# Optimization experiments

Measured on AMD Instinct MI355X. Metric: run time of the kernel, lower is better.

The kernel has to match this reference:

```python
import jax, jax.numpy as jnp
import numpy as np
import math

T_STEPS = 100      # diffusion steps
TED = 16           # time_embed_dim
NODE_C = 4         # node_num_classes
EDGE_C = 2         # edge_num_classes
HID = 64           # hidden_dim
H = 4              # nhead
B = 256            # graphs per batch
NPG = 64           # nodes per graph
DEG = 8            # avg out-degree
N = B * NPG
E = N * DEG
IN_CH = NODE_C + TED  # 20


def sinusoidal_embedding(t_vec, dim):
    # t_vec: [1] float. Matches get_sinusoidal_embedding for even dim.
    half = dim // 2
    scale = math.log(10000.0) / (half - 1)
    freqs = jnp.exp(-jnp.arange(half, dtype=jnp.float32) * scale)  # [half]
    emb = t_vec[:, None] * freqs[None, :]                          # [1, half]
    return jnp.concatenate([jnp.sin(emb), jnp.cos(emb)], axis=1)   # [1, dim]


def transformer_conv(x, src, dst, Wq, bq, Wk, bk, Wv, bv, Ws, bs):
    # PyG TransformerConv, concat=False (mean over heads), root_weight=True,
    # beta=False, no edge features, dropout=0 (eval).
    n = x.shape[0]
    q = (x @ Wq + bq).reshape(n, H, HID)
    k = (x @ Wk + bk).reshape(n, H, HID)
    v = (x @ Wv + bv).reshape(n, H, HID)
    # attention logits per edge, softmax over incoming edges of each dst node
    logits = jnp.sum(q[dst] * k[src], axis=-1) / math.sqrt(HID)    # [E, H]
    lmax = jax.ops.segment_max(logits, dst, num_segments=n)       # [n, H]
    ex = jnp.exp(logits - lmax[dst])                              # [E, H]
    denom = jax.ops.segment_sum(ex, dst, num_segments=n)          # [n, H]
    attn = ex / jnp.where(denom == 0, 1.0, denom)[dst]            # [E, H]
    msg = v[src] * attn[:, :, None]                               # [E, H, HID]
    agg = jax.ops.segment_sum(msg, dst, num_segments=n)           # [n, H, HID]
    return agg.mean(axis=1) + x @ Ws + bs                         # [n, HID]


def setup_inputs() -> dict:
    key = jax.random.key(0)
    ks = jax.random.split(key, 32)

    # node features: random one-hot labels
    labels = jax.random.randint(ks[0], (N,), 0, NODE_C)
    x = jax.nn.one_hot(labels, NODE_C, dtype=jnp.float32)

    # per-graph random edges (kept within each graph via offsets)
    src_l = jax.random.randint(ks[1], (B, NPG * DEG), 0, NPG)
    dst_l = jax.random.randint(ks[2], (B, NPG * DEG), 0, NPG)
    off = (jnp.arange(B) * NPG)[:, None]
    edge_index = jnp.stack([(src_l + off).reshape(-1), (dst_l + off).reshape(-1)]).astype(jnp.int64)

    batch = jnp.repeat(jnp.arange(B, dtype=jnp.int64), NPG)

    def lin(k, fin, fout):
        kw, kb = jax.random.split(k)
        W = jax.random.normal(kw, (fin, fout), jnp.float32) / math.sqrt(fin)
        b = jax.random.normal(kb, (fout,), jnp.float32) * 0.01
        return W, b

    W_time, b_time = lin(ks[3], TED, TED)
    Wq1, bq1 = lin(ks[4], IN_CH, H * HID)
    Wk1, bk1 = lin(ks[5], IN_CH, H * HID)
    Wv1, bv1 = lin(ks[6], IN_CH, H * HID)
    Ws1, bs1 = lin(ks[7], IN_CH, HID)
    Wq2, bq2 = lin(ks[8], HID, H * HID)
    Wk2, bk2 = lin(ks[9], HID, H * HID)
    Wv2, bv2 = lin(ks[10], HID, H * HID)
    Ws2, bs2 = lin(ks[11], HID, HID)
    W_node, b_node = lin(ks[12], HID, NODE_C)
    W_e1, b_e1 = lin(ks[13], 2 * HID, HID)
    W_e2, b_e2 = lin(ks[14], HID, EDGE_C)

    return dict(x=x, edge_index=edge_index, batch=batch, t=50,
                W_time=W_time, b_time=b_time,
                Wq1=Wq1, bq1=bq1, Wk1=Wk1, bk1=bk1, Wv1=Wv1, bv1=bv1, Ws1=Ws1, bs1=bs1,
                Wq2=Wq2, bq2=bq2, Wk2=Wk2, bk2=bk2, Wv2=Wv2, bv2=bv2, Ws2=Ws2, bs2=bs2,
                W_node=W_node, b_node=b_node, W_e1=W_e1, b_e1=b_e1, W_e2=W_e2, b_e2=b_e2)


def reference(x, edge_index, batch, t,
              W_time, b_time,
              Wq1, bq1, Wk1, bk1, Wv1, bv1, Ws1, bs1,
              Wq2, bq2, Wk2, bk2, Wv2, bv2, Ws2, bs2,
              W_node, b_node, W_e1, b_e1, W_e2, b_e2):
    src, dst = edge_index[0], edge_index[1]

    # time embedding: sinusoidal(t/T) -> Linear -> broadcast to all nodes
    t_vec = jnp.asarray([t], jnp.float32) / T_STEPS
    temb = sinusoidal_embedding(t_vec, TED) @ W_time + b_time      # [1, TED]
    temb = jnp.broadcast_to(temb, (x.shape[0], TED))
    x_in = jnp.concatenate([x, temb], axis=1)                      # [N, 20]

    h = jax.nn.relu(transformer_conv(x_in, src, dst, Wq1, bq1, Wk1, bk1, Wv1, bv1, Ws1, bs1))
    h = jax.nn.relu(transformer_conv(h, src, dst, Wq2, bq2, Wk2, bk2, Wv2, bv2, Ws2, bs2))

    node_logits = h @ W_node + b_node                              # [N, 4]

    # to_dense_batch with equal-sized graphs == reshape; vectorized edge MLP
    hd = h.reshape(B, NPG, HID)
    pair = jnp.concatenate([
        jnp.broadcast_to(hd[:, :, None, :], (B, NPG, NPG, HID)),
        jnp.broadcast_to(hd[:, None, :, :], (B, NPG, NPG, HID)),
    ], axis=-1)                                                    # [B, n, n, 2*HID]
    e_hidden = jax.nn.relu(pair @ W_e1 + b_e1)
    edge_logits = e_hidden @ W_e2 + b_e2                           # [B, n, n, 2]
    return node_logits, edge_logits
```

## Files before the change

### kernel.cpp

```cpp
#include <hip/hip_runtime.h>
#include <math.h>

constexpr int EPG  = 512;
constexpr int ETOT = 131072;

constexpr size_t TAB_Q  = 0;
constexpr size_t TAB_K  = 1024;
constexpr size_t TAB_V  = 2048;
constexpr size_t TAB_S  = 3072;
constexpr size_t TAB_LG = 3328;
constexpr size_t TAB_VV = 3392;
constexpr size_t OFF_H2P = 65536;

constexpr int PK_V_HI   = 0;
constexpr int PK_V_LO   = 16384;
constexpr int PK_S_HI   = 32768;
constexpr int PK_S_LO   = 36864;
constexpr int PK_E1T_HI = 40960;
constexpr int PK_E1T_LO = 45056;
constexpr int PK_E1B_HI = 49152;
constexpr int PK_E1B_LO = 53248;
constexpr int PK_M_HI   = 57344;
constexpr int PK_M_LO   = 73728;

typedef short bf16x8 __attribute__((ext_vector_type(8)));
typedef float f32x4  __attribute__((ext_vector_type(4)));

__device__ __forceinline__ short f2bf(float x) {
    unsigned u = __float_as_uint(x);
    u = (u + 0x7fffu + ((u >> 16) & 1u)) >> 16;
    return (short)u;
}
__device__ __forceinline__ float bf2f(short h) {
    return __uint_as_float(((unsigned)(unsigned short)h) << 16);
}
__device__ __forceinline__ void splt(float x, short& hi, short& lo) {
    hi = f2bf(x);
    lo = f2bf(x - bf2f(hi));
}

__device__ __forceinline__ f32x4 mfma3(bf16x8 ah, bf16x8 al, bf16x8 bh, bf16x8 bl, f32x4 c) {
    c = __builtin_amdgcn_mfma_f32_16x16x32_bf16(ah, bh, c, 0, 0, 0);
    c = __builtin_amdgcn_mfma_f32_16x16x32_bf16(ah, bl, c, 0, 0, 0);
    c = __builtin_amdgcn_mfma_f32_16x16x32_bf16(al, bh, c, 0, 0, 0);
    return c;
}

__device__ __forceinline__ bf16x8 ldsfrag(const short* p, int rowb, int kb, int lane) {
    return *(const bf16x8*)&p[(rowb + (lane & 15)) * 72 + kb + ((lane >> 4) << 3)];
}
__device__ __forceinline__ bf16x8 gpfrag(const short* p, int colb, int kb, int lane) {
    return *(const bf16x8*)&p[((colb + (lane & 15)) << 6) + kb + ((lane >> 4) << 3)];
}

__device__ __forceinline__ void unpack8(const unsigned* p, bf16x8& hv, bf16x8& lv) {
    uint4 a = *(const uint4*)p;
    uint4 b = *(const uint4*)(p + 4);
    unsigned u[8] = {a.x, a.y, a.z, a.w, b.x, b.y, b.z, b.w};
    bf16x8 h, l;
    #pragma unroll
    for (int i = 0; i < 8; i++) { h[i] = (short)(u[i] >> 16); l[i] = (short)(u[i] & 0xffffu); }
    hv = h; lv = l;
}

__global__ __launch_bounds__(256) void k_tabprep(
    const int* __restrict__ t_ptr,
    const float* __restrict__ Wt,  const float* __restrict__ bt,
    const float* __restrict__ Wq1, const float* __restrict__ bq1,
    const float* __restrict__ Wk1, const float* __restrict__ bk1,
    const float* __restrict__ Wv1, const float* __restrict__ bv1,
    const float* __restrict__ Ws1, const float* __restrict__ bs1,
    const float* __restrict__ Wq2, const float* __restrict__ bq2,
    const float* __restrict__ Wk2, const float* __restrict__ Wv2,
    const float* __restrict__ Ws2, const float* __restrict__ We1,
    float* __restrict__ ws, short* __restrict__ wsh)
{
    const int t = threadIdx.x, b = blockIdx.x;
    if (b < 112) {
        const float* src; int N; int dhi; int nb;
        if (b < 64)      { src = Wv2;           N = 256; dhi = PK_V_HI;   nb = b; }
        else if (b < 80) { src = Ws2;           N = 64;  dhi = PK_S_HI;   nb = b - 64; }
        else if (b < 96) { src = We1;           N = 64;  dhi = PK_E1T_HI; nb = b - 80; }
        else             { src = We1 + 64 * 64; N = 64;  dhi = PK_E1B_HI; nb = b - 96; }
        int dlo = dhi + N * 64;
        int n = nb * 4 + (t >> 6), kk = t & 63;
        float v = src[(size_t)kk * N + n];
        short hi, lo; splt(v, hi, lo);
        wsh[dhi + n * 64 + kk] = hi;
        wsh[dlo + n * 64 + kk] = lo;
// ... 8 lines not shown
            wk[r][a] = Wk2[(size_t)r * 256 + h * 64 + a];
        }
        __syncthreads();
        int m = t >> 2, k0 = (t & 3) * 16;
        for (int kk = k0; kk < k0 + 16; kk++) {
            float acc = 0.f;
            for (int a = 0; a < 64; a++) acc += wq[kk][a] * wk[m][a];
            acc *= 0.125f;
            short hi, lo; splt(acc, hi, lo);
            wsh[PK_M_HI + h * 4096 + m * 64 + kk] = hi;
            wsh[PK_M_LO + h * 4096 + m * 64 + kk] = lo;
        }
        if (t < 64) {
            float acc = 0.f;
            for (int a = 0; a < 64; a++) acc += wk[t][a] * bq2[h * 64 + a];
            ws[TAB_VV + h * 64 + t] = 0.125f * acc;
        }
        return;
    }
    __shared__ float se[16], temb[16];
    __shared__ float q1t[4][256], k1t[4][256], v1t[4][256], s1t[4][64];
    if (t < 8) {
        float tv = (float)(*t_ptr) * 0.01f;
        float scale = logf(10000.0f) / 7.0f;
        float e = tv * expf(-(float)t * scale);
        se[t]     = sinf(e);
        se[t + 8] = cosf(e);
    }
    __syncthreads();
    if (t < 16) {
        float acc = bt[t];
// ... 23 lines not shown
    }
    __syncthreads();
    for (int idx = t; idx < 1024; idx += 256) {
        int c = idx >> 8, o = idx & 255;
        ws[TAB_Q + idx] = q1t[c][o];
        ws[TAB_K + idx] = k1t[c][o];
        ws[TAB_V + idx] = v1t[c][o];
    }
    ws[TAB_S + t] = s1t[t >> 6][t & 63];
    if (t < 64) {
        int cd = t >> 4, cs = (t >> 2) & 3, h = t & 3;
        float acc = 0.f;
        for (int d = 0; d < 64; d++) acc += q1t[cd][h * 64 + d] * k1t[cs][h * 64 + d];
        ws[TAB_LG + t] = acc * 0.125f;
    }
}

__global__ __launch_bounds__(512, 4) void k_main(
    const float* __restrict__ x, const int* __restrict__ ei,
    const float* __restrict__ ws, const short* __restrict__ wsh,
    const float* __restrict__ bv, const float* __restrict__ bsk,
    unsigned* __restrict__ h2p)
{
    __shared__ __align__(16) char smem[61184];
    short* hHi  = (short*)(smem);
    short* hLo  = (short*)(smem + 9216);
    short* GHi  = (short*)(smem + 18432);
    short* GLo  = (short*)(smem + 23040);
    short* VtHi = (short*)(smem + 27648);
    short* VtLo = (short*)(smem + 36864);
    float* SPf  = (float*)(smem + 46080);
    int*   Cc   = (int*)(smem + 54784);
    float* wcol = (float*)(smem + 59136);
    float* vvs  = (float*)(smem + 60160);
    float* v1t    = (float*)(smem + 27648);
    float* s1t    = (float*)(smem + 31744);
    float* lgs    = (float*)(smem + 32768);
    float* alphaF = (float*)(smem + 33024);
    int*   cls    = (int*)(smem + 37120);
    int*   cnt4   = (int*)(smem + 37376);

    const int g   = blockIdx.x >> 1;
    const int r0  = (blockIdx.x & 1) * 32;
    const int t   = threadIdx.x;
    const int lane = t & 63, w = t >> 6;
    const int rb  = (w & 1) * 16;
    const int cb  = (w >> 1) * 16;
    const int db  = (w & 3) * 16;
    const int jb0 = (w >> 2) * 32;
    const int lg4 = ((lane >> 4) << 2);
    const int lg8 = ((lane >> 4) << 3);
    const int l15 = lane & 15;
    const int row8 = t >> 3;
    const int d08  = (t & 7) * 8;

    for (int i = t; i < 1024; i += 512) v1t[i] = ws[TAB_V + i];
    if (t < 256) s1t[t] = ws[TAB_S + t];
    if (t < 64)  lgs[t] = ws[TAB_LG + t];
    if (t < 256) vvs[t] = ws[TAB_VV + t];
    if (t < 64) {
        const float* xr = x + (size_t)(g * 64 + t) * 4;
        int c = 0;
        if (xr[1] > 0.5f) c = 1;
        if (xr[2] > 0.5f) c = 2;
        if (xr[3] > 0.5f) c = 3;
        cls[t] = c;
    }
    if (t < 256) cnt4[t] = 0;
    for (int i = t; i < 1056; i += 512) Cc[i] = 0;
    __syncthreads();

    {
        int ge = g * EPG + t;
        int ls = ei[ge] - g * 64;
        int ld = ei[ETOT + ge] - g * 64;
        atomicAdd(&cnt4[ld * 4 + cls[ls]], 1);
        int lr = ld - r0;
        if ((unsigned)lr < 32u) {
            int idx = lr * 66 + ls;
            atomicAdd(&Cc[idx >> 1], 1 << ((idx & 1) * 16));
        }
    }
    __syncthreads();

    if (t < 256) {
        int n = t >> 2, h = t & 3;
        int cd = cls[n];
        int   c[4]; float l[4];
        #pragma unroll
        for (int cc = 0; cc < 4; cc++) {
            c[cc] = cnt4[n * 4 + cc];
            l[cc] = lgs[cd * 16 + cc * 4 + h];
        }
        float m = -1e30f;
        #pragma unroll
        for (int cc = 0; cc < 4; cc++) if (c[cc] > 0) m = fmaxf(m, l[cc]);
        float e[4]; float den = 0.f;
        #pragma unroll
        for (int cc = 0; cc < 4; cc++) {
            e[cc] = (c[cc] > 0) ? (float)c[cc] * __expf(l[cc] - m) : 0.f;
            den += e[cc];
        }
        float inv = (den > 0.f) ? 0.25f / den : 0.f;
        #pragma unroll
        for (int cc = 0; cc < 4; cc++) alphaF[n * 16 + h * 4 + cc] = e[cc] * inv;
    }
    __syncthreads();

    {
        int cd = cls[row8];
        float a[16];
        #pragma unroll
        for (int q = 0; q < 16; q++) a[q] = alphaF[row8 * 16 + q];
        #pragma unroll
        for (int jj = 0; jj < 8; jj++) {
            int d = d08 + jj;
            float acc = s1t[cd * 64 + d];
            #pragma unroll
            for (int h = 0; h < 4; h++)
                #pragma unroll
                for (int c = 0; c < 4; c++)
                    acc += a[h * 4 + c] * v1t[c * 256 + h * 64 + d];
            float o = fmaxf(acc, 0.f);
            short hi, lo; splt(o, hi, lo);
            hHi[row8 * 72 + d] = hi;
            hLo[row8 * 72 + d] = lo;
        }
    }
    __syncthreads();

    bf16x8 AhQ0 = ldsfrag(hHi, r0 + rb, 0, lane),  AhQ1 = ldsfrag(hHi, r0 + rb, 32, lane);
    bf16x8 AlQ0 = ldsfrag(hLo, r0 + rb, 0, lane),  AlQ1 = ldsfrag(hLo, r0 + rb, 32, lane);
    bf16x8 sb0h = ldsfrag(hHi, cb, 0, lane),  sb0l = ldsfrag(hLo, cb, 0, lane);
    bf16x8 sb1h = ldsfrag(hHi, cb, 32, lane), sb1l = ldsfrag(hLo, cb, 32, lane);

    if (t < 256) {
        int j = t >> 2, hh = t & 3;
        float acc = 0.f;
        #pragma unroll 8
        for (int k = 0; k < 64; k++)
            acc += (bf2f(hHi[j * 72 + k]) + bf2f(hLo[j * 72 + k])) * vvs[hh * 64 + k];
        wcol[hh * 64 + j] = acc;
    }

    f32x4 skacc = {0.f, 0.f, 0.f, 0.f};
    {
        bf16x8 s0h = gpfrag(wsh + PK_S_HI, cb, 0, lane),  s0l = gpfrag(wsh + PK_S_LO, cb, 0, lane);
        bf16x8 s1h = gpfrag(wsh + PK_S_HI, cb, 32, lane), s1l = gpfrag(wsh + PK_S_LO, cb, 32, lane);
        skacc = mfma3(AhQ0, AlQ0, s0h, s0l, skacc);
        skacc = mfma3(AhQ1, AlQ1, s1h, s1l, skacc);
        float bb = bsk[cb + l15];
        #pragma unroll
        for (int r = 0; r < 4; r++) skacc[r] += bb;
    }

    float hacc[4] = {0.f, 0.f, 0.f, 0.f};
    #pragma unroll 1
    for (int h = 0; h < 4; h++) {
        const short* pmh = wsh + PK_M_HI + h * 4096;
        const short* pml = wsh + PK_M_LO + h * 4096;
        bf16x8 m0h = gpfrag(pmh, cb, 0, lane),  m0l = gpfrag(pml, cb, 0, lane);
        bf16x8 m1h = gpfrag(pmh, cb, 32, lane), m1l = gpfrag(pml, cb, 32, lane);
        int gc0 = h * 64 + db;
        bf16x8 va0h = gpfrag(wsh + PK_V_HI, gc0, 0, lane),  va0l = gpfrag(wsh + PK_V_LO, gc0, 0, lane);
        bf16x8 va1h = gpfrag(wsh + PK_V_HI, gc0, 32, lane), va1l = gpfrag(wsh + PK_V_LO, gc0, 32, lane);
        float4 bv4 = *(const float4*)&bv[gc0 + lg4];
        bf16x8 hb00 = ldsfrag(hHi, jb0, 0, lane),       hb00l = ldsfrag(hLo, jb0, 0, lane);
        bf16x8 hb01 = ldsfrag(hHi, jb0, 32, lane),      hb01l = ldsfrag(hLo, jb0, 32, lane);
        bf16x8 hb10 = ldsfrag(hHi, jb0 + 16, 0, lane),  hb10l = ldsfrag(hLo, jb0 + 16, 0, lane);
        bf16x8 hb11 = ldsfrag(hHi, jb0 + 16, 32, lane), hb11l = ldsfrag(hLo, jb0 + 16, 32, lane);

        {
            f32x4 ga = {0.f, 0.f, 0.f, 0.f};
            ga = mfma3(AhQ0, AlQ0, m0h, m0l, ga);
            ga = mfma3(AhQ1, AlQ1, m1h, m1l, ga);
            int cc = cb + l15;
            #pragma unroll
            for (int r = 0; r < 4; r++) {
                short hi, lo; splt(ga[r], hi, lo);
                GHi[(rb + lg4 + r) * 72 + cc] = hi;
                GLo[(rb + lg4 + r) * 72 + cc] = lo;
            }
        }
        {
            f32x4 vt0 = {0.f, 0.f, 0.f, 0.f}, vt1 = {0.f, 0.f, 0.f, 0.f};
            vt0 = mfma3(va0h, va0l, hb00, hb00l, vt0);
            vt0 = mfma3(va1h, va1l, hb01, hb01l, vt0);
            vt1 = mfma3(va0h, va0l, hb10, hb10l, vt1);
            vt1 = mfma3(va1h, va1l, hb11, hb11l, vt1);
            #pragma unroll
            for (int r = 0; r < 4; r++) {
                int rr = (db + lg4 + r) * 72;
                short hi, lo;
                splt(vt0[r] + bv4[r], hi, lo);
                VtHi[rr + jb0 + l15] = hi;      VtLo[rr + jb0 + l15] = lo;
                splt(vt1[r] + bv4[r], hi, lo);
                VtHi[rr + jb0 + 16 + l15] = hi; VtLo[rr + jb0 + 16 + l15] = lo;
            }
        }
        __syncthreads();

        bf16x8 vb0h = ldsfrag(VtHi, cb, 0, lane),  vb0l = ldsfrag(VtLo, cb, 0, lane);
        bf16x8 vb1h = ldsfrag(VtHi, cb, 32, lane), vb1l = ldsfrag(VtLo, cb, 32, lane);
        {
            bf16x8 g0h = ldsfrag(GHi, rb, 0, lane),  g0l = ldsfrag(GLo, rb, 0, lane);
            bf16x8 g1h = ldsfrag(GHi, rb, 32, lane), g1l = ldsfrag(GLo, rb, 32, lane);
            f32x4 s = {0.f, 0.f, 0.f, 0.f};
            s = mfma3(g0h, g0l, sb0h, sb0l, s);
            s = mfma3(g1h, g1l, sb1h, sb1l, s);
            int cc = cb + l15;
            #pragma unroll
            for (int r = 0; r < 4; r++)
                SPf[(rb + lg4 + r) * 68 + cc] = s[r];
        }
        __syncthreads();

        {
            const int lr = rb + l15;
            float sv[16];
            {
                float4 a0 = *(const float4*)&SPf[lr * 68 + lg8];
                float4 a1 = *(const float4*)&SPf[lr * 68 + lg8 + 4];
                float4 a2 = *(const float4*)&SPf[lr * 68 + 32 + lg8];
                float4 a3 = *(const float4*)&SPf[lr * 68 + 32 + lg8 + 4];
                sv[0]=a0.x; sv[1]=a0.y; sv[2]=a0.z; sv[3]=a0.w;
                sv[4]=a1.x; sv[5]=a1.y; sv[6]=a1.z; sv[7]=a1.w;
                sv[8]=a2.x; sv[9]=a2.y; sv[10]=a2.z; sv[11]=a2.w;
                sv[12]=a3.x; sv[13]=a3.y; sv[14]=a3.z; sv[15]=a3.w;
            }
            int cv[16];
            #pragma unroll
            for (int e = 0; e < 8; e++) {
                int i0 = lr * 66 + lg8 + e;
                int i1 = lr * 66 + 32 + lg8 + e;
                cv[e]     = (Cc[i0 >> 1] >> ((i0 & 1) * 16)) & 0xffff;
                cv[8 + e] = (Cc[i1 >> 1] >> ((i1 & 1) * 16)) & 0xffff;
                sv[e]     += wcol[h * 64 + lg8 + e];
                sv[8 + e] += wcol[h * 64 + 32 + lg8 + e];
            }
            float m = -1e30f;
            #pragma unroll
            for (int e = 0; e < 16; e++) if (cv[e] > 0) m = fmaxf(m, sv[e]);
            m = fmaxf(m, __shfl_xor(m, 16));
            m = fmaxf(m, __shfl_xor(m, 32));
            float den = 0.f; float p[16];
            #pragma unroll
            for (int e = 0; e < 16; e++) {
                p[e] = (cv[e] > 0) ? (float)cv[e] * __expf(sv[e] - m) : 0.f;
                den += p[e];
            }
            den += __shfl_xor(den, 16);
            den += __shfl_xor(den, 32);
            float inv = (den > 0.f) ? 1.f / den : 0.f;
            bf16x8 pa0h, pa0l, pa1h, pa1l;
            #pragma unroll
            for (int e = 0; e < 8; e++) {
                short hi, lo;
                splt(p[e] * inv, hi, lo);      pa0h[e] = hi; pa0l[e] = lo;
                splt(p[8 + e] * inv, hi, lo);  pa1h[e] = hi; pa1l[e] = lo;
            }
            f32x4 pv = {0.f, 0.f, 0.f, 0.f};
            pv = mfma3(pa0h, pa0l, vb0h, vb0l, pv);
            pv = mfma3(pa1h, pa1l, vb1h, vb1l, pv);
            #pragma unroll
            for (int r = 0; r < 4; r++) hacc[r] += pv[r];
        }
        __syncthreads();
    }

    {
        int cc = cb + l15;
        #pragma unroll
        for (int r = 0; r < 4; r++) {
            float v = fmaxf(0.25f * hacc[r] + skacc[r], 0.f);
            short hi, lo; splt(v, hi, lo);
            unsigned u = ((unsigned)(unsigned short)hi << 16) | (unsigned short)(unsigned short)lo;
            h2p[(size_t)(g * 64 + r0 + rb + lg4 + r) * 64 + cc] = u;
        }
    }
}

__global__ __launch_bounds__(512, 4) void k_edge(
    const short* __restrict__ wsh, const unsigned* __restrict__ h2g,
    const float* __restrict__ Wn, const float* __restrict__ bn,
    const float* __restrict__ be1, const float* __restrict__ We2,
    const float* __restrict__ be2, float* __restrict__ out)
{
    __shared__ __align__(16) char smem[45056];
    unsigned* h2P = (unsigned*)(smem);
    float* Af   = (float*)(smem + 17408);
    float* BTf  = (float*)(smem + 26112);
    float* WnS  = (float*)(smem + 43520);
    float* w2s  = (float*)(smem + 44544);

    const int g  = blockIdx.x >> 1;
    const int r0 = (blockIdx.x & 1) * 32;
    const int t  = threadIdx.x;
    const int lane = t & 63, w = t >> 6;
    const int rowbF = (w & 3) * 16, chF = w >> 2;
    const int rbQ = (w & 1) * 16,   cqQ = (w >> 1) * 16;
    const int lg4 = ((lane >> 4) << 2);
    const int lg8 = ((lane >> 4) << 3);
    const int l15 = lane & 15;

    {
        int row = t >> 3, c8 = (t & 7) * 8;
        uint4 a = *(const uint4*)&h2g[(size_t)(g * 64 + row) * 64 + c8];
        uint4 b = *(const uint4*)&h2g[(size_t)(g * 64 + row) * 64 + c8 + 4];
        *(uint4*)&h2P[row * 68 + c8]     = a;
        *(uint4*)&h2P[row * 68 + c8 + 4] = b;
    }
    if (t < 256) WnS[t] = Wn[t];
    if (t < 128) w2s[(t & 1) * 64 + (t >> 1)] = We2[t];
    __syncthreads();

    {
        bf16x8 e0h = gpfrag(wsh + PK_E1T_HI, cqQ, 0, lane),  e0l = gpfrag(wsh + PK_E1T_LO, cqQ, 0, lane);
        bf16x8 e1h = gpfrag(wsh + PK_E1T_HI, cqQ, 32, lane), e1l = gpfrag(wsh + PK_E1T_LO, cqQ, 32, lane);
        bf16x8 aq0, lq0, aq1, lq1;
        unpack8(&h2P[(r0 + rbQ + l15) * 68 + lg8], aq0, lq0);
        unpack8(&h2P[(r0 + rbQ + l15) * 68 + 32 + lg8], aq1, lq1);
        f32x4 aa = {0.f, 0.f, 0.f, 0.f};
        aa = mfma3(aq0, lq0, e0h, e0l, aa);
        aa = mfma3(aq1, lq1, e1h, e1l, aa);
        float bev = be1[cqQ + l15];
        #pragma unroll
        for (int r = 0; r < 4; r++)
            Af[(rbQ + lg4 + r) * 68 + cqQ + l15] = aa[r] + bev;
    }
    {
        bf16x8 af0, lf0, af1, lf1;
        unpack8(&h2P[(rowbF + l15) * 68 + lg8], af0, lf0);
        unpack8(&h2P[(rowbF + l15) * 68 + 32 + lg8], af1, lf1);
        #pragma unroll
        for (int ct = 0; ct < 2; ct++) {
            int colb = chF * 32 + ct * 16;
            bf16x8 b0h = gpfrag(wsh + PK_E1B_HI, colb, 0, lane),  b0l = gpfrag(wsh + PK_E1B_LO, colb, 0, lane);
            bf16x8 b1h = gpfrag(wsh + PK_E1B_HI, colb, 32, lane), b1l = gpfrag(wsh + PK_E1B_LO, colb, 32, lane);
            f32x4 bb = {0.f, 0.f, 0.f, 0.f};
            bb = mfma3(af0, lf0, b0h, b0l, bb);
            bb = mfma3(af1, lf1, b1h, b1l, bb);
            int cc = colb + l15;
            #pragma unroll
            for (int r = 0; r < 4; r++)
                BTf[cc * 68 + rowbF + lg4 + r] = bb[r];
        }
    }
    if (t < 128) {
        int n = t >> 2, c = t & 3;
        float acc = bn[c];
        #pragma unroll 8
        for (int k = 0; k < 64; k++) {
            unsigned u = h2P[(r0 + n) * 68 + k];
            float val = __uint_as_float(u & 0xffff0000u) + __uint_as_float(u << 16);
            acc += val * WnS[k * 4 + c];
        }
        out[(size_t)(g * 64 + r0 + n) * 4 + c] = acc;
    }
    __syncthreads();

    {
        const int wv = t >> 6, j = t & 63;
        float e0[4], e1[4];
        const float cb0 = be2[0], cb1 = be2[1];
        #pragma unroll
        for (int ii = 0; ii < 4; ii++) { e0[ii] = cb0; e1[ii] = cb1; }
        for (int kb = 0; kb < 4; kb++) {
            const int k0 = kb * 16;
            float bj[16], wa[16], wb[16];
            #pragma unroll
            for (int q = 0; q < 16; q++) {
                bj[q] = BTf[(k0 + q) * 68 + j];
                wa[q] = w2s[k0 + q];
                wb[q] = w2s[64 + k0 + q];
            }
            #pragma unroll
            for (int ii = 0; ii < 4; ii++) {
                const float* ar = &Af[(wv * 4 + ii) * 68 + k0];
                #pragma unroll
                for (int q = 0; q < 16; q += 4) {
                    float4 a4 = *(const float4*)(ar + q);
                    float s;
                    s = fmaxf(a4.x + bj[q + 0], 0.f); e0[ii] += s * wa[q + 0]; e1[ii] += s * wb[q + 0];
                    s = fmaxf(a4.y + bj[q + 1], 0.f); e0[ii] += s * wa[q + 1]; e1[ii] += s * wb[q + 1];
                    s = fmaxf(a4.z + bj[q + 2], 0.f); e0[ii] += s * wa[q + 2]; e1[ii] += s * wb[q + 2];
                    s = fmaxf(a4.w + bj[q + 3], 0.f); e0[ii] += s * wa[q + 3]; e1[ii] += s * wb[q + 3];
                }
            }
        }
        float2* oe = (float2*)(out + 65536);
        #pragma unroll
        for (int ii = 0; ii < 4; ii++)
            oe[(size_t)(g * 64 + r0 + wv * 4 + ii) * 64 + j] = make_float2(e0[ii], e1[ii]);
    }
}

extern "C" void kernel_launch(void* const* d_in, const int* in_sizes, int n_in,
                              void* d_out, int out_size, void* d_ws, size_t ws_size,
                              hipStream_t stream)
{
    const float* x    = (const float*)d_in[0];
    const int*   ei   = (const int*)d_in[1];
    const int*   tptr = (const int*)d_in[3];
    const float* Wt   = (const float*)d_in[4];
    const float* bt   = (const float*)d_in[5];
    const float* Wq1  = (const float*)d_in[6];
    const float* bq1  = (const float*)d_in[7];
    const float* Wk1  = (const float*)d_in[8];
// ... 10 lines not shown
    const float* Ws2  = (const float*)d_in[20];
    const float* bs2  = (const float*)d_in[21];
    const float* Wn   = (const float*)d_in[22];
    const float* bn   = (const float*)d_in[23];
    const float* We1  = (const float*)d_in[24];
    const float* be1  = (const float*)d_in[25];
    const float* We2  = (const float*)d_in[26];
    const float* be2  = (const float*)d_in[27];

    float* ws  = (float*)d_ws;
    short* wsh = (short*)(ws + 4096);
    unsigned* h2p = (unsigned*)(ws + OFF_H2P);
    float* out = (float*)d_out;

    k_tabprep<<<117, 256, 0, stream>>>(tptr, Wt, bt, Wq1, bq1, Wk1, bk1, Wv1, bv1,
                                       Ws1, bs1, Wq2, bq2, Wk2, Wv2, Ws2, We1, ws, wsh);
    k_main<<<512, 512, 0, stream>>>(x, ei, ws, wsh, bv2, bs2, h2p);
    k_edge<<<512, 512, 0, stream>>>(wsh, h2p, Wn, bn, be1, We2, be2, out);
}
```

Measured before the change: 65.82 us.

## Prefetch next-head weights, MFMA-ize small GEMVs, and retile edge kernel

In k_main, the per-head M/V weight fragments are prefetched one iteration ahead, which removes one barrier per head. The alpha table is computed in registers instead of shared memory, the wcol GEMV is moved onto MFMA using packed split weights, and G is stored packed with 8-bit adjacency counts. k_edge now runs 1024 blocks of 256 threads, each covering 16 rows, and its node-logit projection uses MFMA with a padded Wn table built in tabprep. Together these aim to cut LDS traffic, barriers and scalar loops, at the cost of more registers and 8-bit count saturation if a node pair has 256 or more edges.

```diff
diff --git a/kernel.cpp b/kernel.cpp
--- a/kernel.cpp
+++ b/kernel.cpp
@@ -9,7 +9,6 @@
 constexpr size_t TAB_V  = 2048;
 constexpr size_t TAB_S  = 3072;
 constexpr size_t TAB_LG = 3328;
-constexpr size_t TAB_VV = 3392;
 constexpr size_t OFF_H2P = 65536;
 
 constexpr int PK_V_HI   = 0;
@@ -22,6 +21,10 @@
 constexpr int PK_E1B_LO = 53248;
 constexpr int PK_M_HI   = 57344;
 constexpr int PK_M_LO   = 73728;
+constexpr int PK_VV_HI  = 90112;
+constexpr int PK_VV_LO  = 91136;
+constexpr int PK_N_HI   = 92160;
+constexpr int PK_N_LO   = 93184;
 
 typedef short bf16x8 __attribute__((ext_vector_type(8)));
 typedef float f32x4  __attribute__((ext_vector_type(4)));
@@ -37,6 +40,10 @@
 __device__ __forceinline__ void splt(float x, short& hi, short& lo) {
     hi = f2bf(x);
     lo = f2bf(x - bf2f(hi));
+}
+__device__ __forceinline__ unsigned packsplt(float x) {
+    short hi, lo; splt(x, hi, lo);
+    return ((unsigned)(unsigned short)hi << 16) | (unsigned short)lo;
 }
 
 __device__ __forceinline__ f32x4 mfma3(bf16x8 ah, bf16x8 al, bf16x8 bh, bf16x8 bl, f32x4 c) {
@@ -52,7 +59,6 @@
 __device__ __forceinline__ bf16x8 gpfrag(const short* p, int colb, int kb, int lane) {
     return *(const bf16x8*)&p[((colb + (lane & 15)) << 6) + kb + ((lane >> 4) << 3)];
 }
-
 __device__ __forceinline__ void unpack8(const unsigned* p, bf16x8& hv, bf16x8& lv) {
     uint4 a = *(const uint4*)p;
     uint4 b = *(const uint4*)(p + 4);
@@ -73,6 +79,7 @@
     const float* __restrict__ Wq2, const float* __restrict__ bq2,
     const float* __restrict__ Wk2, const float* __restrict__ Wv2,
     const float* __restrict__ Ws2, const float* __restrict__ We1,
+    const float* __restrict__ Wn,
     float* __restrict__ ws, short* __restrict__ wsh)
 {
     const int t = threadIdx.x, b = blockIdx.x;
@@ -111,7 +118,9 @@
         if (t < 64) {
             float acc = 0.f;
             for (int a = 0; a < 64; a++) acc += wk[t][a] * bq2[h * 64 + a];
-            ws[TAB_VV + h * 64 + t] = 0.125f * acc;
+            short hi, lo; splt(0.125f * acc, hi, lo);
+            wsh[PK_VV_HI + h * 64 + t] = hi;
+            wsh[PK_VV_LO + h * 64 + t] = lo;
         }
         return;
     }
@@ -165,6 +174,17 @@
         for (int d = 0; d < 64; d++) acc += q1t[cd][h * 64 + d] * k1t[cs][h * 64 + d];
         ws[TAB_LG + t] = acc * 0.125f;
     }
+    for (int idx = t; idx < 1024; idx += 256) {
+        int c = idx >> 6, k = idx & 63;
+        float v = (c < 4) ? Wn[k * 4 + c] : 0.f;
+        short hi, lo; splt(v, hi, lo);
+        wsh[PK_N_HI + idx] = hi;
+        wsh[PK_N_LO + idx] = lo;
+    }
+    for (int idx = 256 + t; idx < 1024; idx += 256) {
+        wsh[PK_VV_HI + idx] = 0;
+        wsh[PK_VV_LO + idx] = 0;
+    }
 }
 
 __global__ __launch_bounds__(512, 4) void k_main(
@@ -173,42 +193,52 @@
     const float* __restrict__ bv, const float* __restrict__ bsk,
     unsigned* __restrict__ h2p)
 {
-    __shared__ __align__(16) char smem[61184];
-    short* hHi  = (short*)(smem);
-    short* hLo  = (short*)(smem + 9216);
-    short* GHi  = (short*)(smem + 18432);
-    short* GLo  = (short*)(smem + 23040);
-    short* VtHi = (short*)(smem + 27648);
-    short* VtLo = (short*)(smem + 36864);
-    float* SPf  = (float*)(smem + 46080);
-    int*   Cc   = (int*)(smem + 54784);
-    float* wcol = (float*)(smem + 59136);
-    float* vvs  = (float*)(smem + 60160);
-    float* v1t    = (float*)(smem + 27648);
-    float* s1t    = (float*)(smem + 31744);
-    float* lgs    = (float*)(smem + 32768);
-    float* alphaF = (float*)(smem + 33024);
-    int*   cls    = (int*)(smem + 37120);
-    int*   cnt4   = (int*)(smem + 37376);
-
-    const int g   = blockIdx.x >> 1;
-    const int r0  = (blockIdx.x & 1) * 32;
-    const int t   = threadIdx.x;
+    __shared__ __align__(16) char smem[59008];
+    short*    hHi  = (short*)(smem);
+    short*    hLo  = (short*)(smem + 9216);
+    short*    VtHi = (short*)(smem + 18432);
+    short*    VtLo = (short*)(smem + 27648);
+    unsigned* Gst  = (unsigned*)(smem + 36864);
+    float*    SPf  = (float*)(smem + 45568);
+    char*     Cc   = (char*)(smem + 54272);
+    float*    wcol = (float*)(smem + 56448);
+    float*    lgs  = (float*)(smem + 57472);
+    int*      cls  = (int*)(smem + 57728);
+    int*      cnt4 = (int*)(smem + 57984);
+    float*    v1t  = (float*)(smem + 18432);
+    float*    s1t  = (float*)(smem + 22528);
+
+    const int g    = blockIdx.x >> 1;
+    const int r0   = (blockIdx.x & 1) * 32;
+    const int t    = threadIdx.x;
     const int lane = t & 63, w = t >> 6;
-    const int rb  = (w & 1) * 16;
-    const int cb  = (w >> 1) * 16;
-    const int db  = (w & 3) * 16;
-    const int jb0 = (w >> 2) * 32;
-    const int lg4 = ((lane >> 4) << 2);
-    const int lg8 = ((lane >> 4) << 3);
-    const int l15 = lane & 15;
+    const int rb   = (w & 1) * 16;
+    const int cb   = (w >> 1) * 16;
+    const int db   = (w & 3) * 16;
+    const int jb0  = (w >> 2) * 32;
+    const int lg4  = ((lane >> 4) << 2);
+    const int lg8  = ((lane >> 4) << 3);
+    const int l15  = lane & 15;
     const int row8 = t >> 3;
     const int d08  = (t & 7) * 8;
+
+    bf16x8 cm0h = gpfrag(wsh + PK_M_HI, cb, 0, lane);
+    bf16x8 cm0l = gpfrag(wsh + PK_M_LO, cb, 0, lane);
+    bf16x8 cm1h = gpfrag(wsh + PK_M_HI, cb, 32, lane);
+    bf16x8 cm1l = gpfrag(wsh + PK_M_LO, cb, 32, lane);
+    bf16x8 cv0h = gpfrag(wsh + PK_V_HI, db, 0, lane);
+    bf16x8 cv0l = gpfrag(wsh + PK_V_LO, db, 0, lane);
+    bf16x8 cv1h = gpfrag(wsh + PK_V_HI, db, 32, lane);
+    bf16x8 cv1l = gpfrag(wsh + PK_V_LO, db, 32, lane);
+    float4 cbv  = *(const float4*)&bv[db + lg4];
+    bf16x8 sk0h = gpfrag(wsh + PK_S_HI, cb, 0, lane);
+    bf16x8 sk0l = gpfrag(wsh + PK_S_LO, cb, 0, lane);
+    bf16x8 sk1h = gpfrag(wsh + PK_S_HI, cb, 32, lane);
+    bf16x8 sk1l = gpfrag(wsh + PK_S_LO, cb, 32, lane);
 
     for (int i = t; i < 1024; i += 512) v1t[i] = ws[TAB_V + i];
     if (t < 256) s1t[t] = ws[TAB_S + t];
     if (t < 64)  lgs[t] = ws[TAB_LG + t];
-    if (t < 256) vvs[t] = ws[TAB_VV + t];
     if (t < 64) {
         const float* xr = x + (size_t)(g * 64 + t) * 4;
         int c = 0;
@@ -218,7 +248,7 @@
         cls[t] = c;
     }
     if (t < 256) cnt4[t] = 0;
-    for (int i = t; i < 1056; i += 512) Cc[i] = 0;
+    for (int i = t; i < 544; i += 512) ((int*)Cc)[i] = 0;
     __syncthreads();
 
     {
@@ -228,50 +258,44 @@
         atomicAdd(&cnt4[ld * 4 + cls[ls]], 1);
         int lr = ld - r0;
         if ((unsigned)lr < 32u) {
-            int idx = lr * 66 + ls;
-            atomicAdd(&Cc[idx >> 1], 1 << ((idx & 1) * 16));
-        }
-    }
-    __syncthreads();
-
-    if (t < 256) {
-        int n = t >> 2, h = t & 3;
-        int cd = cls[n];
-        int   c[4]; float l[4];
-        #pragma unroll
-        for (int cc = 0; cc < 4; cc++) {
-            c[cc] = cnt4[n * 4 + cc];
-            l[cc] = lgs[cd * 16 + cc * 4 + h];
-        }
-        float m = -1e30f;
-        #pragma unroll
-        for (int cc = 0; cc < 4; cc++) if (c[cc] > 0) m = fmaxf(m, l[cc]);
-        float e[4]; float den = 0.f;
-        #pragma unroll
-        for (int cc = 0; cc < 4; cc++) {
-            e[cc] = (c[cc] > 0) ? (float)c[cc] * __expf(l[cc] - m) : 0.f;
-            den += e[cc];
-        }
-        float inv = (den > 0.f) ? 0.25f / den : 0.f;
-        #pragma unroll
-        for (int cc = 0; cc < 4; cc++) alphaF[n * 16 + h * 4 + cc] = e[cc] * inv;
+            int idx = lr * 68 + ls;
+            atomicAdd((int*)(Cc + (idx & ~3)), 1 << ((idx & 3) * 8));
+        }
     }
     __syncthreads();
 
     {
         int cd = cls[row8];
+        int c0 = cnt4[row8 * 4], c1 = cnt4[row8 * 4 + 1],
+            c2 = cnt4[row8 * 4 + 2], c3 = cnt4[row8 * 4 + 3];
         float a[16];
         #pragma unroll
-        for (int q = 0; q < 16; q++) a[q] = alphaF[row8 * 16 + q];
+        for (int hh = 0; hh < 4; hh++) {
+            float l0 = lgs[cd * 16 + hh], l1 = lgs[cd * 16 + 4 + hh],
+                  l2 = lgs[cd * 16 + 8 + hh], l3 = lgs[cd * 16 + 12 + hh];
+            float m = -1e30f;
+            if (c0 > 0) m = fmaxf(m, l0);
+            if (c1 > 0) m = fmaxf(m, l1);
+            if (c2 > 0) m = fmaxf(m, l2);
+            if (c3 > 0) m = fmaxf(m, l3);
+            float e0 = (c0 > 0) ? (float)c0 * __expf(l0 - m) : 0.f;
+            float e1 = (c1 > 0) ? (float)c1 * __expf(l1 - m) : 0.f;
+            float e2 = (c2 > 0) ? (float)c2 * __expf(l2 - m) : 0.f;
+            float e3 = (c3 > 0) ? (float)c3 * __expf(l3 - m) : 0.f;
+            float den = e0 + e1 + e2 + e3;
+            float inv = (den > 0.f) ? 0.25f / den : 0.f;
+            a[hh * 4 + 0] = e0 * inv; a[hh * 4 + 1] = e1 * inv;
+            a[hh * 4 + 2] = e2 * inv; a[hh * 4 + 3] = e3 * inv;
+        }
         #pragma unroll
         for (int jj = 0; jj < 8; jj++) {
             int d = d08 + jj;
             float acc = s1t[cd * 64 + d];
             #pragma unroll
-            for (int h = 0; h < 4; h++)
+            for (int hh = 0; hh < 4; hh++)
                 #pragma unroll
                 for (int c = 0; c < 4; c++)
-                    acc += a[h * 4 + c] * v1t[c * 256 + h * 64 + d];
+                    acc += a[hh * 4 + c] * v1t[c * 256 + hh * 64 + d];
             float o = fmaxf(acc, 0.f);
             short hi, lo; splt(o, hi, lo);
             hHi[row8 * 72 + d] = hi;
@@ -282,70 +306,61 @@
 
     bf16x8 AhQ0 = ldsfrag(hHi, r0 + rb, 0, lane),  AhQ1 = ldsfrag(hHi, r0 + rb, 32, lane);
     bf16x8 AlQ0 = ldsfrag(hLo, r0 + rb, 0, lane),  AlQ1 = ldsfrag(hLo, r0 + rb, 32, lane);
-    bf16x8 sb0h = ldsfrag(hHi, cb, 0, lane),  sb0l = ldsfrag(hLo, cb, 0, lane);
-    bf16x8 sb1h = ldsfrag(hHi, cb, 32, lane), sb1l = ldsfrag(hLo, cb, 32, lane);
-
-    if (t < 256) {
-        int j = t >> 2, hh = t & 3;
-        float acc = 0.f;
-        #pragma unroll 8
-        for (int k = 0; k < 64; k++)
-            acc += (bf2f(hHi[j * 72 + k]) + bf2f(hLo[j * 72 + k])) * vvs[hh * 64 + k];
-        wcol[hh * 64 + j] = acc;
-    }
 
     f32x4 skacc = {0.f, 0.f, 0.f, 0.f};
-    {
-        bf16x8 s0h = gpfrag(wsh + PK_S_HI, cb, 0, lane),  s0l = gpfrag(wsh + PK_S_LO, cb, 0, lane);
-        bf16x8 s1h = gpfrag(wsh + PK_S_HI, cb, 32, lane), s1l = gpfrag(wsh + PK_S_LO, cb, 32, lane);
-        skacc = mfma3(AhQ0, AlQ0, s0h, s0l, skacc);
-        skacc = mfma3(AhQ1, AlQ1, s1h, s1l, skacc);
+    skacc = mfma3(AhQ0, AlQ0, sk0h, sk0l, skacc);
+    skacc = mfma3(AhQ1, AlQ1, sk1h, sk1l, skacc);
+    {
         float bb = bsk[cb + l15];
         #pragma unroll
         for (int r = 0; r < 4; r++) skacc[r] += bb;
     }
 
+    if (w < 4) {
+        bf16x8 vv0h = gpfrag(wsh + PK_VV_HI, 0, 0, lane);
+        bf16x8 vv0l = gpfrag(wsh + PK_VV_LO, 0, 0, lane);
+        bf16x8 vv1h = gpfrag(wsh + PK_VV_HI, 0, 32, lane);
+        bf16x8 vv1l = gpfrag(wsh + PK_VV_LO, 0, 32, lane);
+        bf16x8 a0h = ldsfrag(hHi, w * 16, 0, lane),  a1h = ldsfrag(hHi, w * 16, 32, lane);
+        bf16x8 a0l = ldsfrag(hLo, w * 16, 0, lane),  a1l = ldsfrag(hLo, w * 16, 32, lane);
+        f32x4 wc = {0.f, 0.f, 0.f, 0.f};
+        wc = mfma3(a0h, a0l, vv0h, vv0l, wc);
+        wc = mfma3(a1h, a1l, vv1h, vv1l, wc);
+        if (l15 < 4) {
+            #pragma unroll
+            for (int r = 0; r < 4; r++)
+                wcol[l15 * 64 + w * 16 + lg4 + r] = wc[r];
+        }
+    }
+
     float hacc[4] = {0.f, 0.f, 0.f, 0.f};
     #pragma unroll 1
     for (int h = 0; h < 4; h++) {
-        const short* pmh = wsh + PK_M_HI + h * 4096;
-        const short* pml = wsh + PK_M_LO + h * 4096;
-        bf16x8 m0h = gpfrag(pmh, cb, 0, lane),  m0l = gpfrag(pml, cb, 0, lane);
-        bf16x8 m1h = gpfrag(pmh, cb, 32, lane), m1l = gpfrag(pml, cb, 32, lane);
-        int gc0 = h * 64 + db;
-        bf16x8 va0h = gpfrag(wsh + PK_V_HI, gc0, 0, lane),  va0l = gpfrag(wsh + PK_V_LO, gc0, 0, lane);
-        bf16x8 va1h = gpfrag(wsh + PK_V_HI, gc0, 32, lane), va1l = gpfrag(wsh + PK_V_LO, gc0, 32, lane);
-        float4 bv4 = *(const float4*)&bv[gc0 + lg4];
-        bf16x8 hb00 = ldsfrag(hHi, jb0, 0, lane),       hb00l = ldsfrag(hLo, jb0, 0, lane);
-        bf16x8 hb01 = ldsfrag(hHi, jb0, 32, lane),      hb01l = ldsfrag(hLo, jb0, 32, lane);
-        bf16x8 hb10 = ldsfrag(hHi, jb0 + 16, 0, lane),  hb10l = ldsfrag(hLo, jb0 + 16, 0, lane);
-        bf16x8 hb11 = ldsfrag(hHi, jb0 + 16, 32, lane), hb11l = ldsfrag(hLo, jb0 + 16, 32, lane);
-
         {
             f32x4 ga = {0.f, 0.f, 0.f, 0.f};
-            ga = mfma3(AhQ0, AlQ0, m0h, m0l, ga);
-            ga = mfma3(AhQ1, AlQ1, m1h, m1l, ga);
-            int cc = cb + l15;
-            #pragma unroll
-            for (int r = 0; r < 4; r++) {
-                short hi, lo; splt(ga[r], hi, lo);
-                GHi[(rb + lg4 + r) * 72 + cc] = hi;
-                GLo[(rb + lg4 + r) * 72 + cc] = lo;
-            }
+            ga = mfma3(AhQ0, AlQ0, cm0h, cm0l, ga);
+            ga = mfma3(AhQ1, AlQ1, cm1h, cm1l, ga);
+            #pragma unroll
+            for (int r = 0; r < 4; r++)
+                Gst[(rb + lg4 + r) * 68 + cb + l15] = packsplt(ga[r]);
         }
         {
+            bf16x8 hb00h = ldsfrag(hHi, jb0, 0, lane),       hb00l = ldsfrag(hLo, jb0, 0, lane);
+            bf16x8 hb01h = ldsfrag(hHi, jb0, 32, lane),      hb01l = ldsfrag(hLo, jb0, 32, lane);
+            bf16x8 hb10h = ldsfrag(hHi, jb0 + 16, 0, lane),  hb10l = ldsfrag(hLo, jb0 + 16, 0, lane);
+            bf16x8 hb11h = ldsfrag(hHi, jb0 + 16, 32, lane), hb11l = ldsfrag(hLo, jb0 + 16, 32, lane);
             f32x4 vt0 = {0.f, 0.f, 0.f, 0.f}, vt1 = {0.f, 0.f, 0.f, 0.f};
-            vt0 = mfma3(va0h, va0l, hb00, hb00l, vt0);
-            vt0 = mfma3(va1h, va1l, hb01, hb01l, vt0);
-            vt1 = mfma3(va0h, va0l, hb10, hb10l, vt1);
-            vt1 = mfma3(va1h, va1l, hb11, hb11l, vt1);
+            vt0 = mfma3(cv0h, cv0l, hb00h, hb00l, vt0);
+            vt0 = mfma3(cv1h, cv1l, hb01h, hb01l, vt0);
+            vt1 = mfma3(cv0h, cv0l, hb10h, hb10l, vt1);
+            vt1 = mfma3(cv1h, cv1l, hb11h, hb11l, vt1);
             #pragma unroll
             for (int r = 0; r < 4; r++) {
                 int rr = (db + lg4 + r) * 72;
                 short hi, lo;
-                splt(vt0[r] + bv4[r], hi, lo);
+                splt(vt0[r] + cbv[r], hi, lo);
                 VtHi[rr + jb0 + l15] = hi;      VtLo[rr + jb0 + l15] = lo;
-                splt(vt1[r] + bv4[r], hi, lo);
+                splt(vt1[r] + cbv[r], hi, lo);
                 VtHi[rr + jb0 + 16 + l15] = hi; VtLo[rr + jb0 + 16 + l15] = lo;
             }
         }
@@ -354,164 +369,187 @@
         bf16x8 vb0h = ldsfrag(VtHi, cb, 0, lane),  vb0l = ldsfrag(VtLo, cb, 0, lane);
         bf16x8 vb1h = ldsfrag(VtHi, cb, 32, lane), vb1l = ldsfrag(VtLo, cb, 32, lane);
         {
-            bf16x8 g0h = ldsfrag(GHi, rb, 0, lane),  g0l = ldsfrag(GLo, rb, 0, lane);
-            bf16x8 g1h = ldsfrag(GHi, rb, 32, lane), g1l = ldsfrag(GLo, rb, 32, lane);
+            bf16x8 gh0, gl0, gh1, gl1;
+            const unsigned* gp = Gst + (rb + l15) * 68 + lg8;
+            unpack8(gp, gh0, gl0);
+            unpack8(gp + 32, gh1, gl1);
+            bf16x8 sb0h = ldsfrag(hHi, cb, 0, lane),  sb0l = ldsfrag(hLo, cb, 0, lane);
+            bf16x8 sb1h = ldsfrag(hHi, cb, 32, lane), sb1l = ldsfrag(hLo, cb, 32, lane);
             f32x4 s = {0.f, 0.f, 0.f, 0.f};
-            s = mfma3(g0h, g0l, sb0h, sb0l, s);
-            s = mfma3(g1h, g1l, sb1h, sb1l, s);
-            int cc = cb + l15;
+            s = mfma3(gh0, gl0, sb0h, sb0l, s);
+            s = mfma3(gh1, gl1, sb1h, sb1l, s);
             #pragma unroll
             for (int r = 0; r < 4; r++)
-                SPf[(rb + lg4 + r) * 68 + cc] = s[r];
-        }
-        __syncthreads();
-
+                SPf[(rb + lg4 + r) * 68 + cb + l15] = s[r];
+        }
         {
-            const int lr = rb + l15;
-            float sv[16];
+            int hn = (h + 1) & 3;
+            const short* pmh = wsh + PK_M_HI + hn * 4096;
+            const short* pml = wsh + PK_M_LO + hn * 4096;
+            bf16x8 nm0h = gpfrag(pmh, cb, 0, lane),  nm0l = gpfrag(pml, cb, 0, lane);
+            bf16x8 nm1h = gpfrag(pmh, cb, 32, lane), nm1l = gpfrag(pml, cb, 32, lane);
+            int gc = hn * 64 + db;
+            bf16x8 nv0h = gpfrag(wsh + PK_V_HI, gc, 0, lane);
+            bf16x8 nv0l = gpfrag(wsh + PK_V_LO, gc, 0, lane);
+            bf16x8 nv1h = gpfrag(wsh + PK_V_HI, gc, 32, lane);
+            bf16x8 nv1l = gpfrag(wsh + PK_V_LO, gc, 32, lane);
+            float4 nbv  = *(const float4*)&bv[gc + lg4];
+            __syncthreads();
+
             {
-                float4 a0 = *(const float4*)&SPf[lr * 68 + lg8];
-                float4 a1 = *(const float4*)&SPf[lr * 68 + lg8 + 4];
-                float4 a2 = *(const float4*)&SPf[lr * 68 + 32 + lg8];
-                float4 a3 = *(const float4*)&SPf[lr * 68 + 32 + lg8 + 4];
-                sv[0]=a0.x; sv[1]=a0.y; sv[2]=a0.z; sv[3]=a0.w;
-                sv[4]=a1.x; sv[5]=a1.y; sv[6]=a1.z; sv[7]=a1.w;
-                sv[8]=a2.x; sv[9]=a2.y; sv[10]=a2.z; sv[11]=a2.w;
-                sv[12]=a3.x; sv[13]=a3.y; sv[14]=a3.z; sv[15]=a3.w;
+                const int lr = rb + l15;
+                float sv[16];
+                {
+                    const float* sp = SPf + lr * 68;
+                    float4 a0 = *(const float4*)(sp + lg8);
+                    float4 a1 = *(const float4*)(sp + lg8 + 4);
+                    float4 a2 = *(const float4*)(sp + 32 + lg8);
+                    float4 a3 = *(const float4*)(sp + 32 + lg8 + 4);
+                    sv[0]=a0.x; sv[1]=a0.y; sv[2]=a0.z; sv[3]=a0.w;
+                    sv[4]=a1.x; sv[5]=a1.y; sv[6]=a1.z; sv[7]=a1.w;
+                    sv[8]=a2.x; sv[9]=a2.y; sv[10]=a2.z; sv[11]=a2.w;
+                    sv[12]=a3.x; sv[13]=a3.y; sv[14]=a3.z; sv[15]=a3.w;
+                }
+                int cv[16];
+                {
+                    const unsigned* crow = (const unsigned*)(Cc + lr * 68);
+                    unsigned c0 = crow[lg8 >> 2], c1 = crow[(lg8 >> 2) + 1];
+                    unsigned c2 = crow[(32 + lg8) >> 2], c3 = crow[((32 + lg8) >> 2) + 1];
+                    #pragma unroll
+                    for (int e = 0; e < 4; e++) {
+                        cv[e]      = (c0 >> (e * 8)) & 255;
+                        cv[4 + e]  = (c1 >> (e * 8)) & 255;
+                        cv[8 + e]  = (c2 >> (e * 8)) & 255;
+                        cv[12 + e] = (c3 >> (e * 8)) & 255;
+                    }
+                }
+                #pragma unroll
+                for (int e = 0; e < 8; e++) {
+                    sv[e]     += wcol[h * 64 + lg8 + e];
+                    sv[8 + e] += wcol[h * 64 + 32 + lg8 + e];
+                }
+                float m = -1e30f;
+                #pragma unroll
+                for (int e = 0; e < 16; e++) if (cv[e] > 0) m = fmaxf(m, sv[e]);
+                m = fmaxf(m, __shfl_xor(m, 16));
+                m = fmaxf(m, __shfl_xor(m, 32));
+                float den = 0.f; float p[16];
+                #pragma unroll
+                for (int e = 0; e < 16; e++) {
+                    p[e] = (cv[e] > 0) ? (float)cv[e] * __expf(sv[e] - m) : 0.f;
+                    den += p[e];
+                }
+                den += __shfl_xor(den, 16);
+                den += __shfl_xor(den, 32);
+                float inv = (den > 0.f) ? 1.f / den : 0.f;
+                bf16x8 pa0h, pa0l, pa1h, pa1l;
+                #pragma unroll
+                for (int e = 0; e < 8; e++) {
+                    short hi, lo;
+                    splt(p[e] * inv, hi, lo);      pa0h[e] = hi; pa0l[e] = lo;
+                    splt(p[8 + e] * inv, hi, lo);  pa1h[e] = hi; pa1l[e] = lo;
+                }
+                f32x4 pv = {0.f, 0.f, 0.f, 0.f};
+                pv = mfma3(pa0h, pa0l, vb0h, vb0l, pv);
+                pv = mfma3(pa1h, pa1l, vb1h, vb1l, pv);
+                #pragma unroll
+                for (int r = 0; r < 4; r++) hacc[r] += pv[r];
             }
-            int cv[16];
-            #pragma unroll
-            for (int e = 0; e < 8; e++) {
-                int i0 = lr * 66 + lg8 + e;
-                int i1 = lr * 66 + 32 + lg8 + e;
-                cv[e]     = (Cc[i0 >> 1] >> ((i0 & 1) * 16)) & 0xffff;
-                cv[8 + e] = (Cc[i1 >> 1] >> ((i1 & 1) * 16)) & 0xffff;
-                sv[e]     += wcol[h * 64 + lg8 + e];
-                sv[8 + e] += wcol[h * 64 + 32 + lg8 + e];
-            }
-            float m = -1e30f;
-            #pragma unroll
-            for (int e = 0; e < 16; e++) if (cv[e] > 0) m = fmaxf(m, sv[e]);
-            m = fmaxf(m, __shfl_xor(m, 16));
-            m = fmaxf(m, __shfl_xor(m, 32));
-            float den = 0.f; float p[16];
-            #pragma unroll
-            for (int e = 0; e < 16; e++) {
-                p[e] = (cv[e] > 0) ? (float)cv[e] * __expf(sv[e] - m) : 0.f;
-                den += p[e];
-            }
-            den += __shfl_xor(den, 16);
-            den += __shfl_xor(den, 32);
-            float inv = (den > 0.f) ? 1.f / den : 0.f;
-            bf16x8 pa0h, pa0l, pa1h, pa1l;
-            #pragma unroll
-            for (int e = 0; e < 8; e++) {
-                short hi, lo;
-                splt(p[e] * inv, hi, lo);      pa0h[e] = hi; pa0l[e] = lo;
-                splt(p[8 + e] * inv, hi, lo);  pa1h[e] = hi; pa1l[e] = lo;
-            }
-            f32x4 pv = {0.f, 0.f, 0.f, 0.f};
-            pv = mfma3(pa0h, pa0l, vb0h, vb0l, pv);
-            pv = mfma3(pa1h, pa1l, vb1h, vb1l, pv);
-            #pragma unroll
-            for (int r = 0; r < 4; r++) hacc[r] += pv[r];
-        }
-        __syncthreads();
-    }
-
-    {
-        int cc = cb + l15;
-        #pragma unroll
-        for (int r = 0; r < 4; r++) {
-            float v = fmaxf(0.25f * hacc[r] + skacc[r], 0.f);
-            short hi, lo; splt(v, hi, lo);
-            unsigned u = ((unsigned)(unsigned short)hi << 16) | (unsigned short)(unsigned short)lo;
-            h2p[(size_t)(g * 64 + r0 + rb + lg4 + r) * 64 + cc] = u;
-        }
-    }
-}
-
-__global__ __launch_bounds__(512, 4) void k_edge(
+            cm0h = nm0h; cm0l = nm0l; cm1h = nm1h; cm1l = nm1l;
+            cv0h = nv0h; cv0l = nv0l; cv1h = nv1h; cv1l = nv1l;
+            cbv = nbv;
+        }
+    }
+
+    #pragma unroll
+    for (int r = 0; r < 4; r++) {
+        float v = fmaxf(0.25f * hacc[r] + skacc[r], 0.f);
+        h2p[(size_t)(g * 64 + r0 + rb + lg4 + r) * 64 + cb + l15] = packsplt(v);
+    }
+}
+
+__global__ __launch_bounds__(256, 4) void k_edge(
     const short* __restrict__ wsh, const unsigned* __restrict__ h2g,
-    const float* __restrict__ Wn, const float* __restrict__ bn,
-    const float* __restrict__ be1, const float* __restrict__ We2,
-    const float* __restrict__ be2, float* __restrict__ out)
+    const float* __restrict__ bn, const float* __restrict__ be1,
+    const float* __restrict__ We2, const float* __restrict__ be2,
+    float* __restrict__ out)
 {
-    __shared__ __align__(16) char smem[45056];
+    __shared__ __align__(16) char smem[39680];
     unsigned* h2P = (unsigned*)(smem);
-    float* Af   = (float*)(smem + 17408);
-    float* BTf  = (float*)(smem + 26112);
-    float* WnS  = (float*)(smem + 43520);
-    float* w2s  = (float*)(smem + 44544);
-
-    const int g  = blockIdx.x >> 1;
-    const int r0 = (blockIdx.x & 1) * 32;
+    float*    Af  = (float*)(smem + 17408);
+    float*    BTf = (float*)(smem + 21760);
+    float*    w2s = (float*)(smem + 39168);
+
+    const int g  = blockIdx.x >> 2;
+    const int i0 = (blockIdx.x & 3) * 16;
     const int t  = threadIdx.x;
     const int lane = t & 63, w = t >> 6;
-    const int rowbF = (w & 3) * 16, chF = w >> 2;
-    const int rbQ = (w & 1) * 16,   cqQ = (w >> 1) * 16;
     const int lg4 = ((lane >> 4) << 2);
     const int lg8 = ((lane >> 4) << 3);
     const int l15 = lane & 15;
 
     {
-        int row = t >> 3, c8 = (t & 7) * 8;
-        uint4 a = *(const uint4*)&h2g[(size_t)(g * 64 + row) * 64 + c8];
-        uint4 b = *(const uint4*)&h2g[(size_t)(g * 64 + row) * 64 + c8 + 4];
-        *(uint4*)&h2P[row * 68 + c8]     = a;
-        *(uint4*)&h2P[row * 68 + c8 + 4] = b;
-    }
-    if (t < 256) WnS[t] = Wn[t];
+        int row = t >> 2, c16 = (t & 3) * 16;
+        const unsigned* src = h2g + (size_t)(g * 64 + row) * 64 + c16;
+        #pragma unroll
+        for (int q = 0; q < 4; q++)
+            *(uint4*)&h2P[row * 68 + c16 + q * 4] = *(const uint4*)(src + q * 4);
+    }
     if (t < 128) w2s[(t & 1) * 64 + (t >> 1)] = We2[t];
     __syncthreads();
 
     {
-        bf16x8 e0h = gpfrag(wsh + PK_E1T_HI, cqQ, 0, lane),  e0l = gpfrag(wsh + PK_E1T_LO, cqQ, 0, lane);
-        bf16x8 e1h = gpfrag(wsh + PK_E1T_HI, cqQ, 32, lane), e1l = gpfrag(wsh + PK_E1T_LO, cqQ, 32, lane);
         bf16x8 aq0, lq0, aq1, lq1;
-        unpack8(&h2P[(r0 + rbQ + l15) * 68 + lg8], aq0, lq0);
-        unpack8(&h2P[(r0 + rbQ + l15) * 68 + 32 + lg8], aq1, lq1);
-        f32x4 aa = {0.f, 0.f, 0.f, 0.f};
-        aa = mfma3(aq0, lq0, e0h, e0l, aa);
-        aa = mfma3(aq1, lq1, e1h, e1l, aa);
-        float bev = be1[cqQ + l15];
+        const unsigned* ap = h2P + (i0 + l15) * 68;
+        unpack8(ap + lg8, aq0, lq0);
+        unpack8(ap + 32 + lg8, aq1, lq1);
+        {
+            int colb = w * 16;
+            bf16x8 e0h = gpfrag(wsh + PK_E1T_HI, colb, 0, lane),  e0l = gpfrag(wsh + PK_E1T_LO, colb, 0, lane);
+            bf16x8 e1h = gpfrag(wsh + PK_E1T_HI, colb, 32, lane), e1l = gpfrag(wsh + PK_E1T_LO, colb, 32, lane);
+            f32x4 aa = {0.f, 0.f, 0.f, 0.f};
+            aa = mfma3(aq0, lq0, e0h, e0l, aa);
+            aa = mfma3(aq1, lq1, e1h, e1l, aa);
+            float bev = be1[colb + l15];
+            #pragma unroll
+            for (int r = 0; r < 4; r++)
+                Af[(lg4 + r) * 68 + colb + l15] = aa[r] + bev;
+        }
+        if (w == 0) {
+            bf16x8 n0h = gpfrag(wsh + PK_N_HI, 0, 0, lane),  n0l = gpfrag(wsh + PK_N_LO, 0, 0, lane);
+            bf16x8 n1h = gpfrag(wsh + PK_N_HI, 0, 32, lane), n1l = gpfrag(wsh + PK_N_LO, 0, 32, lane);
+            f32x4 nl = {0.f, 0.f, 0.f, 0.f};
+            nl = mfma3(aq0, lq0, n0h, n0l, nl);
+            nl = mfma3(aq1, lq1, n1h, n1l, nl);
+            if (l15 < 4) {
+                #pragma unroll
+                for (int r = 0; r < 4; r++)
+                    out[(size_t)(g * 64 + i0 + lg4 + r) * 4 + l15] = nl[r] + bn[l15];
+            }
+        }
+    }
+    {
+        bf16x8 af0, lf0, af1, lf1;
+        const unsigned* ap = h2P + (w * 16 + l15) * 68;
+        unpack8(ap + lg8, af0, lf0);
+        unpack8(ap + 32 + lg8, af1, lf1);
         #pragma unroll
-        for (int r = 0; r < 4; r++)
-            Af[(rbQ + lg4 + r) * 68 + cqQ + l15] = aa[r] + bev;
-    }
-    {
-        bf16x8 af0, lf0, af1, lf1;
-        unpack8(&h2P[(rowbF + l15) * 68 + lg8], af0, lf0);
-        unpack8(&h2P[(rowbF + l15) * 68 + 32 + lg8], af1, lf1);
-        #pragma unroll
-        for (int ct = 0; ct < 2; ct++) {
-            int colb = chF * 32 + ct * 16;
+        for (int ct = 0; ct < 4; ct++) {
+            int colb = ct * 16;
             bf16x8 b0h = gpfrag(wsh + PK_E1B_HI, colb, 0, lane),  b0l = gpfrag(wsh + PK_E1B_LO, colb, 0, lane);
             bf16x8 b1h = gpfrag(wsh + PK_E1B_HI, colb, 32, lane), b1l = gpfrag(wsh + PK_E1B_LO, colb, 32, lane);
             f32x4 bb = {0.f, 0.f, 0.f, 0.f};
             bb = mfma3(af0, lf0, b0h, b0l, bb);
             bb = mfma3(af1, lf1, b1h, b1l, bb);
-            int cc = colb + l15;
             #pragma unroll
             for (int r = 0; r < 4; r++)
-                BTf[cc * 68 + rowbF + lg4 + r] = bb[r];
-        }
-    }
-    if (t < 128) {
-        int n = t >> 2, c = t & 3;
-        float acc = bn[c];
-        #pragma unroll 8
-        for (int k = 0; k < 64; k++) {
-            unsigned u = h2P[(r0 + n) * 68 + k];
-            float val = __uint_as_float(u & 0xffff0000u) + __uint_as_float(u << 16);
-            acc += val * WnS[k * 4 + c];
-        }
-        out[(size_t)(g * 64 + r0 + n) * 4 + c] = acc;
-    }
-    __syncthreads();
-
-    {
-        const int wv = t >> 6, j = t & 63;
+                BTf[(colb + l15) * 68 + w * 16 + lg4 + r] = bb[r];
+        }
+    }
+    __syncthreads();
+
+    {
+        const int j = t & 63;
         float e0[4], e1[4];
         const float cb0 = be2[0], cb1 = be2[1];
         #pragma unroll
@@ -527,7 +565,7 @@
             }
             #pragma unroll
             for (int ii = 0; ii < 4; ii++) {
-                const float* ar = &Af[(wv * 4 + ii) * 68 + k0];
+                const float* ar = &Af[(w * 4 + ii) * 68 + k0];
                 #pragma unroll
                 for (int q = 0; q < 16; q += 4) {
                     float4 a4 = *(const float4*)(ar + q);
@@ -542,7 +580,7 @@
         float2* oe = (float2*)(out + 65536);
         #pragma unroll
         for (int ii = 0; ii < 4; ii++)
-            oe[(size_t)(g * 64 + r0 + wv * 4 + ii) * 64 + j] = make_float2(e0[ii], e1[ii]);
+            oe[(size_t)(g * 64 + i0 + w * 4 + ii) * 64 + j] = make_float2(e0[ii], e1[ii]);
     }
 }
 
@@ -583,7 +621,8 @@
     float* out = (float*)d_out;
 
     k_tabprep<<<117, 256, 0, stream>>>(tptr, Wt, bt, Wq1, bq1, Wk1, bk1, Wv1, bv1,
-                                       Ws1, bs1, Wq2, bq2, Wk2, Wv2, Ws2, We1, ws, wsh);
+                                       Ws1, bs1, Wq2, bq2, Wk2, Wv2, Ws2, We1, Wn,
+                                       ws, wsh);
     k_main<<<512, 512, 0, stream>>>(x, ei, ws, wsh, bv2, bs2, h2p);
-    k_edge<<<512, 512, 0, stream>>>(wsh, h2p, Wn, bn, be1, We2, be2, out);
-}
+    k_edge<<<1024, 256, 0, stream>>>(wsh, h2p, bn, be1, We2, be2, out);
+}
```

After: 96.47 us. 1.47x slower.
